# Optimization experiments

Measured on AMD Instinct MI355X. Metric: run time of the kernel, lower is better.

## Reference

```python
import jax, jax.numpy as jnp
import numpy as np

D_MODEL = 2048
N_STATE = 256          # power of two
RANK = 64
LEVELS = int(np.log2(N_STATE))  # 8 butterfly levels
B, S = 4, 4096


def setup_inputs() -> dict:
    key = jax.random.key(0)
    ks = jax.random.split(key, 7)
    u = jax.random.normal(ks[0], (B, S, D_MODEL), dtype=jnp.float32)
    # stacked 2x2 butterfly factors, one per level (orthogonal-ish init)
    A_factors = jax.random.normal(ks[1], (LEVELS, 2, 2), dtype=jnp.float32)
    A_factors = A_factors / jnp.linalg.norm(A_factors, axis=-1, keepdims=True)
    W_b_rank = jax.random.normal(ks[2], (D_MODEL, RANK), dtype=jnp.float32) * (1.0 / np.sqrt(D_MODEL))
    W_b_state = jax.random.normal(ks[3], (RANK, N_STATE), dtype=jnp.float32) * (1.0 / np.sqrt(RANK))
    W_c_rank = jax.random.normal(ks[4], (N_STATE, RANK), dtype=jnp.float32) * (1.0 / np.sqrt(N_STATE))
    W_c_model = jax.random.normal(ks[5], (RANK, D_MODEL), dtype=jnp.float32) * (1.0 / np.sqrt(RANK))
    D_vec = jax.random.normal(ks[6], (D_MODEL,), dtype=jnp.float32) * 0.02
    return {"u": u, "A_factors": A_factors, "W_b_rank": W_b_rank,
            "W_b_state": W_b_state, "W_c_rank": W_c_rank,
            "W_c_model": W_c_model, "D_vec": D_vec}


def _apply_butterfly(state, A_factors):
    # state: [B, S, N]; reshape N into LEVELS axes of size 2 and apply a 2x2
    # factor along each axis (contracting the axis with A's FIRST dim, i.e.
    # x @ A, matching tf.matmul(flattened, factor)).
    b, s, n = state.shape
    x = state.reshape((b, s) + (2,) * LEVELS)
    for lvl in range(LEVELS):
        ax = 2 + lvl
        x = jnp.moveaxis(jnp.tensordot(x, A_factors[lvl], axes=[[ax], [0]]), -1, ax)
    return x.reshape(b, s, n)


def reference(u, A_factors, W_b_rank, W_b_state, W_c_rank, W_c_model, D_vec):
    # B path: low-rank projection to state space
    state = (u @ W_b_rank) @ W_b_state              # [B,S,N]
    # A: butterfly-structured state transform
    state = _apply_butterfly(state, A_factors)      # [B,S,N]
    # C path: low-rank projection back to model dim
    y = (state @ W_c_rank) @ W_c_model              # [B,S,D]
    # D: elementwise feedthrough
    return y + D_vec * u
```

## Files before the change

kernel.cpp:

```cpp
#include <hip/hip_runtime.h>

typedef unsigned short ushort_t;
typedef __attribute__((ext_vector_type(8))) short bf16x8;
typedef __attribute__((ext_vector_type(4))) float f32x4;
typedef __attribute__((ext_vector_type(4))) unsigned short us4;
typedef __attribute__((ext_vector_type(2))) unsigned short us2;

#define DM 2048
#define RK 64

__device__ __forceinline__ ushort_t f2b(float f) {
    union { float f; unsigned u; } x; x.f = f;
    unsigned r = x.u + 0x7fff + ((x.u >> 16) & 1);
    return (ushort_t)(r >> 16);
}

__global__ void k_p1(const float* __restrict__ Wbs, const float* __restrict__ Af,
                     const float* __restrict__ Wcr, float* __restrict__ Mmid) {
    __shared__ float X[64 * 256];
    const int tid = threadIdx.x;
#pragma unroll
    for (int i = 0; i < 16; ++i) {
        int e = (i * 256 + tid) * 4;
        *(float4*)&X[e] = *(const float4*)&Wbs[e];
    }
    __syncthreads();
#pragma unroll
    for (int l = 0; l < 8; ++l) {
        const int bit = 1 << (7 - l);
        const float a00 = Af[l * 4 + 0], a01 = Af[l * 4 + 1];
        const float a10 = Af[l * 4 + 2], a11 = Af[l * 4 + 3];
#pragma unroll 4
        for (int p = 0; p < 32; ++p) {
            int pid = p * 256 + tid;
            int row = pid >> 7;
            int off = pid & 127;
            int lo = off & (bit - 1);
            int n0 = ((off ^ lo) << 1) | lo;
            int n1 = n0 | bit;
            float x0 = X[row * 256 + n0], x1 = X[row * 256 + n1];
            X[row * 256 + n0] = x0 * a00 + x1 * a10;
            X[row * 256 + n1] = x0 * a01 + x1 * a11;
        }
        __syncthreads();
    }
    int g = blockIdx.x * 256 + tid;
    int r1 = g >> 6, r2 = g & 63;
    float s = 0.f;
#pragma unroll 8
    for (int n = 0; n < 256; ++n) s += X[r1 * 256 + n] * Wcr[n * 64 + r2];
    Mmid[g] = s;
}

__global__ void k_p2(const float* __restrict__ Wbr, const float* __restrict__ Mmid,
                     const float* __restrict__ Wcm,
                     ushort_t* __restrict__ WeffT, ushort_t* __restrict__ WcT) {
    const int b = blockIdx.x, tid = threadIdx.x;
    if (b < 32) {
        __shared__ float LW[64][65];
        __shared__ float LM[64 * 64];
#pragma unroll
        for (int i = 0; i < 4; ++i) {
            int e = (i * 256 + tid) * 4;
            int kk = e >> 6, r = e & 63;
            float4 v = *(const float4*)&Wbr[(size_t)b * 4096 + e];
            LW[kk][r] = v.x; LW[kk][r + 1] = v.y; LW[kk][r + 2] = v.z; LW[kk][r + 3] = v.w;
        }
#pragma unroll
        for (int i = 0; i < 4; ++i) {
            int e = (i * 256 + tid) * 4;
            *(float4*)&LM[e] = *(const float4*)&Mmid[e];
        }
        __syncthreads();
        int kk = tid & 63, n0 = (tid >> 6) * 16;
        float acc[16];
#pragma unroll
        for (int j = 0; j < 16; ++j) acc[j] = 0.f;
        for (int r = 0; r < 64; ++r) {
            float wv = LW[kk][r];
            const float* mrow = &LM[r * 64 + n0];
            float4 m0 = *(const float4*)(mrow);
            float4 m1 = *(const float4*)(mrow + 4);
            float4 m2 = *(const float4*)(mrow + 8);
            float4 m3 = *(const float4*)(mrow + 12);
            acc[0] += wv * m0.x; acc[1] += wv * m0.y; acc[2] += wv * m0.z; acc[3] += wv * m0.w;
            acc[4] += wv * m1.x; acc[5] += wv * m1.y; acc[6] += wv * m1.z; acc[7] += wv * m1.w;
            acc[8] += wv * m2.x; acc[9] += wv * m2.y; acc[10] += wv * m2.z; acc[11] += wv * m2.w;
            acc[12] += wv * m3.x; acc[13] += wv * m3.y; acc[14] += wv * m3.z; acc[15] += wv * m3.w;
        }
#pragma unroll
        for (int j = 0; j < 16; ++j)
            WeffT[(size_t)(n0 + j) * DM + b * 64 + kk] = f2b(acc[j]);
    } else {
        __shared__ float LT[64][65];
        const int n0 = (b - 32) * 64;
#pragma unroll
        for (int i = 0; i < 4; ++i) {
            int e = (i * 256 + tid) * 4;
            int k = e >> 6, nn = e & 63;
            float4 v = *(const float4*)&Wcm[(size_t)k * DM + n0 + nn];
            LT[k][nn] = v.x; LT[k][nn + 1] = v.y; LT[k][nn + 2] = v.z; LT[k][nn + 3] = v.w;
        }
        __syncthreads();
#pragma unroll
        for (int i = 0; i < 4; ++i) {
            int e = (i * 256 + tid) * 4;
            int nn = e >> 6, k = e & 63;
            us4 o;
            o.x = f2b(LT[k][nn]); o.y = f2b(LT[k + 1][nn]);
            o.z = f2b(LT[k + 2][nn]); o.w = f2b(LT[k + 3][nn]);
            *(us4*)&WcT[(size_t)(n0 + nn) * RK + k] = o;
        }
    }
}

__global__ __launch_bounds__(512) void k_a(const float* __restrict__ u,
                                           const ushort_t* __restrict__ WeffT,
                                           ushort_t* __restrict__ tg) {
    __shared__ float red[8][64][20];

    const int tid = threadIdx.x;
    const int w = tid >> 6;
    const int lane = tid & 63;
    const int m16 = lane & 15;
    const int quad = lane >> 4;
    const size_t r0 = (size_t)blockIdx.x * 64;

    bf16x8 Wf[8][4];
    {
        const ushort_t* wbase = WeffT + (size_t)m16 * DM + w * 256 + quad * 8;
#pragma unroll
        for (int c = 0; c < 8; ++c)
#pragma unroll
            for (int j = 0; j < 4; ++j)
                Wf[c][j] = *(const bf16x8*)(wbase + (size_t)j * 16 * DM + c * 32);
    }

    for (int g = 0; g < 4; ++g) {
        const float* ap = u + (r0 + g * 16 + m16) * DM + w * 256 + quad * 8;
        f32x4 acc[4];
#pragma unroll
        for (int j = 0; j < 4; ++j) acc[j] = (f32x4){0.f, 0.f, 0.f, 0.f};

#pragma unroll
        for (int c = 0; c < 8; ++c) {
            float4 u0 = *(const float4*)(ap + c * 32);
            float4 u1 = *(const float4*)(ap + c * 32 + 4);
            bf16x8 a;
            a[0] = (short)f2b(u0.x); a[1] = (short)f2b(u0.y);
            a[2] = (short)f2b(u0.z); a[3] = (short)f2b(u0.w);
            a[4] = (short)f2b(u1.x); a[5] = (short)f2b(u1.y);
            a[6] = (short)f2b(u1.z); a[7] = (short)f2b(u1.w);
#pragma unroll
            for (int j = 0; j < 4; ++j)
                acc[j] = __builtin_amdgcn_mfma_f32_16x16x32_bf16(a, Wf[c][j], acc[j], 0, 0, 0);
        }

#pragma unroll
        for (int j = 0; j < 4; ++j)
            *(f32x4*)&red[w][16 * j + m16][quad * 4] = acc[j];
        __syncthreads();

        {
            const int r = tid >> 5;
            const int n0 = (tid & 31) * 2;
            float s0 = 0.f, s1 = 0.f;
#pragma unroll
            for (int ww = 0; ww < 8; ++ww) {
                s0 += red[ww][n0][r];
                s1 += red[ww][n0 + 1][r];
            }
            us2 o; o.x = f2b(s0); o.y = f2b(s1);
            *(us2*)&tg[(r0 + g * 16 + r) * RK + n0] = o;
        }
        __syncthreads();
    }
}

__global__ __launch_bounds__(64) void k_b(const ushort_t* __restrict__ tg,
                                          const float* __restrict__ u,
                                          const ushort_t* __restrict__ WcT,
                                          const float* __restrict__ Dvec,
                                          float* __restrict__ out) {
    const int lane = threadIdx.x;
    const int m16 = lane & 15;
    const int quad = lane >> 4;
    const size_t r0 = (size_t)(blockIdx.x >> 4) * 128;
    const int c0 = (blockIdx.x & 15) * 128;

    bf16x8 wb0[8], wb1[8];
    float4 dvv[8];
#pragma unroll
    for (int ct = 0; ct < 8; ++ct) {
        const ushort_t* p = WcT + (size_t)(c0 + ct * 16 + m16) * RK + quad * 8;
        wb0[ct] = *(const bf16x8*)(p);
        wb1[ct] = *(const bf16x8*)(p + 32);
        dvv[ct] = *(const float4*)(Dvec + c0 + ct * 16 + quad * 4);
    }

    for (int g = 0; g < 8; ++g) {
        const size_t rg = r0 + g * 16;
        const ushort_t* tp = tg + (rg + m16) * RK + quad * 8;
        bf16x8 ta0 = *(const bf16x8*)(tp);
        bf16x8 ta1 = *(const bf16x8*)(tp + 32);
        const float* up = u + (rg + m16) * DM + c0 + quad * 4;
        float* op = out + (rg + m16) * DM + c0 + quad * 4;
#pragma unroll
        for (int ct = 0; ct < 8; ++ct) {
            f32x4 o = {0.f, 0.f, 0.f, 0.f};
            o = __builtin_amdgcn_mfma_f32_16x16x32_bf16(wb0[ct], ta0, o, 0, 0, 0);
            o = __builtin_amdgcn_mfma_f32_16x16x32_bf16(wb1[ct], ta1, o, 0, 0, 0);
            float4 uv = *(const float4*)(up + ct * 16);
            f32x4 st;
            st[0] = o[0] + dvv[ct].x * uv.x;
            st[1] = o[1] + dvv[ct].y * uv.y;
            st[2] = o[2] + dvv[ct].z * uv.z;
            st[3] = o[3] + dvv[ct].w * uv.w;
            *(f32x4*)(op + ct * 16) = st;
        }
    }
}

extern "C" void kernel_launch(void* const* d_in, const int* in_sizes, int n_in,
                              void* d_out, int out_size, void* d_ws, size_t ws_size,
                              hipStream_t stream) {
    (void)in_sizes; (void)n_in; (void)out_size; (void)ws_size;
    const float* u   = (const float*)d_in[0];
    const float* Af  = (const float*)d_in[1];
    const float* Wbr = (const float*)d_in[2];
    const float* Wbs = (const float*)d_in[3];
    const float* Wcr = (const float*)d_in[4];
    const float* Wcm = (const float*)d_in[5];
    const float* Dv  = (const float*)d_in[6];
    float* out = (float*)d_out;

    char* ws = (char*)d_ws;
    float*    Mmid  = (float*)(ws + 0);
    ushort_t* WeffT = (ushort_t*)(ws + 16384);
    ushort_t* WcT   = (ushort_t*)(ws + 278528);
    ushort_t* tg    = (ushort_t*)(ws + 540672);

    k_p1<<<16, 256, 0, stream>>>(Wbs, Af, Wcr, Mmid);
    k_p2<<<64, 256, 0, stream>>>(Wbr, Mmid, Wcm, WeffT, WcT);
    k_a <<<256, 512, 0, stream>>>(u, WeffT, tg);
    k_b <<<2048, 64, 0, stream>>>(tg, u, WcT, Dv, out);
}
```

Before: 319.5 us.

## Fuse down-projection and up-projection kernels via shared-memory rank intermediate

```diff
diff --git a/kernel.cpp b/kernel.cpp
--- a/kernel.cpp
+++ b/kernel.cpp
@@ -114,10 +114,13 @@
     }
 }
 
-__global__ __launch_bounds__(512) void k_a(const float* __restrict__ u,
-                                           const ushort_t* __restrict__ WeffT,
-                                           ushort_t* __restrict__ tg) {
+__global__ __launch_bounds__(512) void k_main(const float* __restrict__ u,
+                                              const ushort_t* __restrict__ WeffT,
+                                              const ushort_t* __restrict__ WcT,
+                                              const float* __restrict__ Dvec,
+                                              float* __restrict__ out) {
     __shared__ float red[8][64][20];
+    __shared__ ushort_t tsh[64 * 72];
 
     const int tid = threadIdx.x;
     const int w = tid >> 6;
@@ -171,52 +174,41 @@
                 s1 += red[ww][n0 + 1][r];
             }
             us2 o; o.x = f2b(s0); o.y = f2b(s1);
-            *(us2*)&tg[(r0 + g * 16 + r) * RK + n0] = o;
-        }
-        __syncthreads();
-    }
-}
-
-__global__ __launch_bounds__(64) void k_b(const ushort_t* __restrict__ tg,
-                                          const float* __restrict__ u,
-                                          const ushort_t* __restrict__ WcT,
-                                          const float* __restrict__ Dvec,
-                                          float* __restrict__ out) {
-    const int lane = threadIdx.x;
-    const int m16 = lane & 15;
-    const int quad = lane >> 4;
-    const size_t r0 = (size_t)(blockIdx.x >> 4) * 128;
-    const int c0 = (blockIdx.x & 15) * 128;
-
-    bf16x8 wb0[8], wb1[8];
-    float4 dvv[8];
-#pragma unroll
-    for (int ct = 0; ct < 8; ++ct) {
-        const ushort_t* p = WcT + (size_t)(c0 + ct * 16 + m16) * RK + quad * 8;
-        wb0[ct] = *(const bf16x8*)(p);
-        wb1[ct] = *(const bf16x8*)(p + 32);
-        dvv[ct] = *(const float4*)(Dvec + c0 + ct * 16 + quad * 4);
-    }
-
-    for (int g = 0; g < 8; ++g) {
-        const size_t rg = r0 + g * 16;
-        const ushort_t* tp = tg + (rg + m16) * RK + quad * 8;
-        bf16x8 ta0 = *(const bf16x8*)(tp);
-        bf16x8 ta1 = *(const bf16x8*)(tp + 32);
-        const float* up = u + (rg + m16) * DM + c0 + quad * 4;
-        float* op = out + (rg + m16) * DM + c0 + quad * 4;
-#pragma unroll
-        for (int ct = 0; ct < 8; ++ct) {
+            *(us2*)&tsh[(g * 16 + r) * 72 + n0] = o;
+        }
+        __syncthreads();
+    }
+
+    bf16x8 ta0[4], ta1[4];
+#pragma unroll
+    for (int rg = 0; rg < 4; ++rg) {
+        ta0[rg] = *(const bf16x8*)&tsh[(rg * 16 + m16) * 72 + quad * 8];
+        ta1[rg] = *(const bf16x8*)&tsh[(rg * 16 + m16) * 72 + 32 + quad * 8];
+    }
+    const int cb = w * 256;
+    const ushort_t* wcb = WcT + (size_t)(cb + m16) * RK + quad * 8;
+    const float* up = u + (r0 + m16) * DM + cb + quad * 4;
+    const float* dp = Dvec + cb + quad * 4;
+    float* op = out + (r0 + m16) * DM + cb + quad * 4;
+
+#pragma unroll 2
+    for (int ct = 0; ct < 16; ++ct) {
+        const ushort_t* p = wcb + (size_t)ct * 16 * RK;
+        bf16x8 wb0 = *(const bf16x8*)(p);
+        bf16x8 wb1 = *(const bf16x8*)(p + 32);
+        float4 dv = *(const float4*)(dp + ct * 16);
+#pragma unroll
+        for (int rg = 0; rg < 4; ++rg) {
             f32x4 o = {0.f, 0.f, 0.f, 0.f};
-            o = __builtin_amdgcn_mfma_f32_16x16x32_bf16(wb0[ct], ta0, o, 0, 0, 0);
-            o = __builtin_amdgcn_mfma_f32_16x16x32_bf16(wb1[ct], ta1, o, 0, 0, 0);
-            float4 uv = *(const float4*)(up + ct * 16);
+            o = __builtin_amdgcn_mfma_f32_16x16x32_bf16(wb0, ta0[rg], o, 0, 0, 0);
+            o = __builtin_amdgcn_mfma_f32_16x16x32_bf16(wb1, ta1[rg], o, 0, 0, 0);
+            float4 uv = *(const float4*)(up + (size_t)rg * 16 * DM + ct * 16);
             f32x4 st;
-            st[0] = o[0] + dvv[ct].x * uv.x;
-            st[1] = o[1] + dvv[ct].y * uv.y;
-            st[2] = o[2] + dvv[ct].z * uv.z;
-            st[3] = o[3] + dvv[ct].w * uv.w;
-            *(f32x4*)(op + ct * 16) = st;
+            st[0] = o[0] + dv.x * uv.x;
+            st[1] = o[1] + dv.y * uv.y;
+            st[2] = o[2] + dv.z * uv.z;
+            st[3] = o[3] + dv.w * uv.w;
+            *(f32x4*)(op + (size_t)rg * 16 * DM + ct * 16) = st;
         }
     }
 }
@@ -238,10 +230,8 @@
     float*    Mmid  = (float*)(ws + 0);
     ushort_t* WeffT = (ushort_t*)(ws + 16384);
     ushort_t* WcT   = (ushort_t*)(ws + 278528);
-    ushort_t* tg    = (ushort_t*)(ws + 540672);
 
     k_p1<<<16, 256, 0, stream>>>(Wbs, Af, Wcr, Mmid);
     k_p2<<<64, 256, 0, stream>>>(Wbr, Mmid, Wcm, WeffT, WcT);
-    k_a <<<256, 512, 0, stream>>>(u, WeffT, tg);
-    k_b <<<2048, 64, 0, stream>>>(tg, u, WcT, Dv, out);
-}
+    k_main<<<256, 512, 0, stream>>>(u, WeffT, WcT, Dv, out);
+}
```

After: 315.5 us. No clear change (-1.2%).
